# Kernel optimization log

Hardware: AMD Instinct MI355X
Metric: run time of the kernel (lower is better)

The kernel has to match this reference:

```python
import jax, jax.numpy as jnp
import numpy as np

NUM_HEADS = 16
ROPE_BASE = 10000.0


def _rope_cos_sin(seq_len, head_dim, dtype):
    # half-split RoPE tables, shape [1, S, 1, head_dim]
    inv_freq = 1.0 / (ROPE_BASE ** (jnp.arange(0, head_dim, 2, dtype=jnp.float32) / head_dim))
    ang = jnp.arange(seq_len, dtype=jnp.float32)[:, None] * inv_freq[None, :]  # [S, hd/2]
    cos = jnp.concatenate([jnp.cos(ang), jnp.cos(ang)], axis=-1)[None, :, None, :]
    sin = jnp.concatenate([jnp.sin(ang), jnp.sin(ang)], axis=-1)[None, :, None, :]
    return cos.astype(dtype), sin.astype(dtype)


def _rotate_half(t):
    h = t.shape[-1] // 2
    return jnp.concatenate([-t[..., h:], t[..., :h]], axis=-1)


def setup_inputs() -> dict:
    key = jax.random.key(0)
    ks = jax.random.split(key, 5)
    B, S, D = 2, 2048, 1024
    std = 1.0 / np.sqrt(D)
    return {
        "x": jax.random.normal(ks[0], (B, S, D), dtype=jnp.float32),
        "Wqkv": jax.random.normal(ks[1], (D, 3 * D), dtype=jnp.float32) * std,
        "bqkv": jax.random.normal(ks[2], (3 * D,), dtype=jnp.float32) * 0.02,
        "Wproj": jax.random.normal(ks[3], (D, D), dtype=jnp.float32) * std,
        "bproj": jax.random.normal(ks[4], (D,), dtype=jnp.float32) * 0.02,
    }


def reference(x, Wqkv, bqkv, Wproj, bproj):
    B, S, D = x.shape
    H = NUM_HEADS
    hd = D // H
    scale = hd ** (-0.5)

    # fused QKV projection, then split: [B, S, 3, H, hd]
    qkv = (jnp.einsum("bsd,de->bse", x, Wqkv) + bqkv).reshape(B, S, 3, H, hd)
    q, k, v = qkv[:, :, 0], qkv[:, :, 1], qkv[:, :, 2]  # each [B, S, H, hd]

    # rotary embedding on q, k
    cos, sin = _rope_cos_sin(S, hd, x.dtype)
    q = q * cos + _rotate_half(q) * sin
    k = k * cos + _rotate_half(k) * sin

    # scaled dot-product attention (non-causal, matching flash-attn default here)
    scores = jnp.einsum("bqhd,bkhd->bhqk", q, k) * scale  # [B, H, S, S]
    probs = jax.nn.softmax(scores, axis=-1)
    o = jnp.einsum("bhqk,bkhd->bqhd", probs, v).reshape(B, S, D)

    # output projection
    return jnp.einsum("bsd,de->bse", o, Wproj) + bproj
```

## Files before the change

kernel.cpp:

```cpp
#include <hip/hip_runtime.h>

typedef unsigned short u16;
typedef unsigned int   u32;
typedef __bf16 bf16x8 __attribute__((ext_vector_type(8)));
typedef float  f32x4  __attribute__((ext_vector_type(4)));
typedef float  f32x16 __attribute__((ext_vector_type(16)));
typedef u32    u32x4  __attribute__((ext_vector_type(4)));

__device__ __forceinline__ u16 f2bf(float f) {
  u32 u = __builtin_bit_cast(u32, f);
  u += 0x7fffu + ((u >> 16) & 1u);
  return (u16)(u >> 16);
}

#define GLOAD_LDS16(gptr, lptr)                                              \
  __builtin_amdgcn_global_load_lds(                                          \
      (const __attribute__((address_space(1))) void*)(gptr),                 \
      (__attribute__((address_space(3))) void*)(lptr), 16, 0, 0)

#define QK_FOLD 0.18033688011112042f

__global__ __launch_bounds__(256) void prep_kernel(const float* __restrict__ x,
                                                   u16* __restrict__ xb,
                                                   const float* __restrict__ Wq,
                                                   u16* __restrict__ Wqt,
                                                   const float* __restrict__ Wp,
                                                   u16* __restrict__ Wpt,
                                                   float* __restrict__ cost,
                                                   float* __restrict__ sint) {
  __shared__ float tile[32][33];
  const int bid = blockIdx.x;
  if (bid < 4096) {
    const int i = bid * 256 + threadIdx.x;
    const float4 v = ((const float4*)x)[i];
    uint2 o;
    o.x = (u32)f2bf(v.x) | ((u32)f2bf(v.y) << 16);
    o.y = (u32)f2bf(v.z) | ((u32)f2bf(v.w) << 16);
    ((uint2*)xb)[i] = o;
  } else if (bid < 8192) {
    const bool isq = bid < 7168;
    const float* W = isq ? Wq : Wp;
    u16* Wt = isq ? Wqt : Wpt;
    const int t = isq ? (bid - 4096) : (bid - 7168);
    const int ntiles = isq ? 96 : 32;
    const int N = isq ? 3072 : 1024;
    const int k0 = (t / ntiles) * 32, n0 = (t % ntiles) * 32;
    const int tx = threadIdx.x & 31, ty = threadIdx.x >> 5;
#pragma unroll
    for (int i = 0; i < 32; i += 8)
      tile[ty + i][tx] = W[(size_t)(k0 + ty + i) * N + n0 + tx];
    __syncthreads();
#pragma unroll
    for (int i = 0; i < 32; i += 8)
      Wt[(size_t)(n0 + ty + i) * 1024 + k0 + tx] = f2bf(tile[tx][ty + i]);
  } else {
    const int idx = (bid - 8192) * 256 + threadIdx.x;
    const int s = idx >> 5, i = idx & 31;
    float inv = exp2f(-13.287712379549449f * (float)i * (1.0f / 32.0f));
    float sn, cs;
    sincosf((float)s * inv, &sn, &cs);
    cost[idx] = cs;
    sint[idx] = sn;
  }
}

__global__ __launch_bounds__(256) void gemm_qkv_rope_kernel(const u16* __restrict__ A,
                                                            const u16* __restrict__ Bt,
                                                            const float* __restrict__ bias,
                                                            const float* __restrict__ cost,
                                                            const float* __restrict__ sint,
                                                            u16* __restrict__ qb,
                                                            u16* __restrict__ kb,
                                                            u16* __restrict__ vt) {
  __shared__ u16 As[128][64];
  __shared__ u16 Bs[128][64];
  const int bm = blockIdx.y, bn = blockIdx.x;
  const int tid = threadIdx.x;
  const int wave = tid >> 6, lane = tid & 63;
  const int wr = wave >> 1, wc = wave & 1;
  const int l15 = lane & 15, lhi = lane >> 4;
  f32x4 acc[4][4] = {};
  const int K = 1024;

  const size_t arow0 = (size_t)bm * 128, brow0 = (size_t)bn * 128;
  const int srow_in = lane >> 3;
  const int sslot   = (lane & 7) ^ srow_in;

  for (int k0 = 0; k0 < K; k0 += 64) {
#pragma unroll
    for (int i = 0; i < 4; i++) {
      const int r = wave * 32 + i * 8 + srow_in;
      GLOAD_LDS16(A  + (arow0 + r) * K + k0 + sslot * 8, &As[wave * 32 + i * 8][0]);
      GLOAD_LDS16(Bt + (brow0 + r) * K + k0 + sslot * 8, &Bs[wave * 32 + i * 8][0]);
    }
    __syncthreads();

    bf16x8 af[4][2], bfr[4][2];
#pragma unroll
    for (int m = 0; m < 4; m++) {
      const int r = wr * 64 + m * 16 + l15;
#pragma unroll
      for (int kk = 0; kk < 2; kk++)
        af[m][kk] = *(const bf16x8*)(&As[0][0] + r * 64 + (((kk * 4 + lhi) ^ (r & 7)) * 8));
    }
#pragma unroll
    for (int n = 0; n < 4; n++) {
      const int r = wc * 64 + n * 16 + l15;
#pragma unroll
      for (int kk = 0; kk < 2; kk++)
        bfr[n][kk] = *(const bf16x8*)(&Bs[0][0] + r * 64 + (((kk * 4 + lhi) ^ (r & 7)) * 8));
    }
#pragma unroll
    for (int m = 0; m < 4; m++)
#pragma unroll
      for (int n = 0; n < 4; n++) {
        acc[m][n] = __builtin_amdgcn_mfma_f32_16x16x32_bf16(af[m][0], bfr[n][0], acc[m][n], 0, 0, 0);
        acc[m][n] = __builtin_amdgcn_mfma_f32_16x16x32_bf16(af[m][1], bfr[n][1], acc[m][n], 0, 0, 0);
      }
    __syncthreads();
  }

  float bv[4];
#pragma unroll
  for (int n = 0; n < 4; n++) bv[n] = bias[bn * 128 + wc * 64 + n * 16 + l15];

  if (bn < 16) {
    const bool isq = bn < 8;
    u16* dst = isq ? qb : kb;
    const int hcol = bn * 2 + wc - (isq ? 0 : 16);
    const float fold = isq ? QK_FOLD : 1.0f;
#pragma unroll
    for (int m = 0; m < 4; m++)
#pragma unroll
      for (int r = 0; r < 4; r++) {
        const int row = bm * 128 + wr * 64 + m * 16 + lhi * 4 + r;
        const int b = row >> 11, s = row & 2047;
        const float cs0 = cost[s * 32 + l15],      sn0 = sint[s * 32 + l15];
        const float cs1 = cost[s * 32 + 16 + l15], sn1 = sint[s * 32 + 16 + l15];
        const float q0 = acc[m][0][r] + bv[0], q1 = acc[m][2][r] + bv[2];
        const float q2 = acc[m][1][r] + bv[1], q3 = acc[m][3][r] + bv[3];
        u16* orow = dst + ((size_t)(b * 16 + hcol) * 2048 + s) * 64;
        orow[l15]      = f2bf((q0 * cs0 - q1 * sn0) * fold);
        orow[l15 + 32] = f2bf((q1 * cs0 + q0 * sn0) * fold);
        orow[l15 + 16] = f2bf((q2 * cs1 - q3 * sn1) * fold);
        orow[l15 + 48] = f2bf((q3 * cs1 + q2 * sn1) * fold);
      }
  } else {
    const int hcol = bn * 2 + wc - 32;
    const int b = bm >> 4;
#pragma unroll
    for (int n = 0; n < 4; n++) {
      const int d = n * 16 + l15;
      u16* dcol = vt + ((size_t)(b * 16 + hcol) * 64 + d) * 2048;
#pragma unroll
      for (int m = 0; m < 4; m++) {
        const int s = (bm * 128 + wr * 64 + m * 16 + lhi * 4) & 2047;
        uint2 w;
        w.x = (u32)f2bf(acc[m][n][0] + bv[n]) | ((u32)f2bf(acc[m][n][1] + bv[n]) << 16);
        w.y = (u32)f2bf(acc[m][n][2] + bv[n]) | ((u32)f2bf(acc[m][n][3] + bv[n]) << 16);
        *(uint2*)(dcol + s) = w;
      }
    }
  }
}

__global__ __launch_bounds__(256) void gemm_bias_m64_kernel(const u16* __restrict__ A,
                                                            const u16* __restrict__ Bt,
                                                            const float* __restrict__ bias,
                                                            float* __restrict__ C,
                                                            int M, int N, int K) {
  __shared__ u16 As[64][64];
  __shared__ u16 Bs[128][64];
  const int bm = blockIdx.y, bn = blockIdx.x;
  const int tid = threadIdx.x;
  const int wave = tid >> 6, lane = tid & 63;
  const int wr = wave >> 1, wc = wave & 1;
  const int l15 = lane & 15, lhi = lane >> 4;
  f32x4 acc[2][4] = {};

  const size_t arow0 = (size_t)bm * 64, brow0 = (size_t)bn * 128;
  const int srow_in = lane >> 3;
  const int sslot   = (lane & 7) ^ srow_in;

  for (int k0 = 0; k0 < K; k0 += 64) {
#pragma unroll
    for (int i = 0; i < 2; i++) {
      const int r = wave * 16 + i * 8 + srow_in;
      GLOAD_LDS16(A + (arow0 + r) * K + k0 + sslot * 8, &As[wave * 16 + i * 8][0]);
    }
#pragma unroll
    for (int i = 0; i < 4; i++) {
      const int r = wave * 32 + i * 8 + srow_in;
      GLOAD_LDS16(Bt + (brow0 + r) * K + k0 + sslot * 8, &Bs[wave * 32 + i * 8][0]);
    }
    __syncthreads();

    bf16x8 af[2][2], bfr[4][2];
#pragma unroll
    for (int m = 0; m < 2; m++) {
      const int r = wr * 32 + m * 16 + l15;
#pragma unroll
      for (int kk = 0; kk < 2; kk++)
        af[m][kk] = *(const bf16x8*)(&As[0][0] + r * 64 + (((kk * 4 + lhi) ^ (r & 7)) * 8));
    }
#pragma unroll
    for (int n = 0; n < 4; n++) {
      const int r = wc * 64 + n * 16 + l15;
#pragma unroll
      for (int kk = 0; kk < 2; kk++)
        bfr[n][kk] = *(const bf16x8*)(&Bs[0][0] + r * 64 + (((kk * 4 + lhi) ^ (r & 7)) * 8));
    }
#pragma unroll
    for (int m = 0; m < 2; m++)
#pragma unroll
      for (int n = 0; n < 4; n++) {
        acc[m][n] = __builtin_amdgcn_mfma_f32_16x16x32_bf16(af[m][0], bfr[n][0], acc[m][n], 0, 0, 0);
        acc[m][n] = __builtin_amdgcn_mfma_f32_16x16x32_bf16(af[m][1], bfr[n][1], acc[m][n], 0, 0, 0);
      }
    __syncthreads();
  }
#pragma unroll
  for (int n = 0; n < 4; n++) {
    int col = bn * 128 + wc * 64 + n * 16 + l15;
    float bvv = bias[col];
#pragma unroll
    for (int m = 0; m < 2; m++)
#pragma unroll
      for (int r = 0; r < 4; r++) {
        int row = bm * 64 + wr * 32 + m * 16 + lhi * 4 + r;
        C[(size_t)row * N + col] = acc[m][n][r] + bvv;
      }
  }
}

__global__ __launch_bounds__(256) void flash_attn_kernel(const u16* __restrict__ qg,
                                                         const u16* __restrict__ kg,
                                                         const u16* __restrict__ vg,
                                                         u16* __restrict__ og) {
  __shared__ u16 Ks[2][64][64];
  __shared__ u16 Vs[2][64][64];
  const int hw = blockIdx.x;
  const int lb = (hw & 7) * 64 + (hw >> 3);
  const int qt = lb & 15, bh = lb >> 4;
  const int b = bh >> 4, h = bh & 15;
  const int tid = threadIdx.x, wave = tid >> 6, lane = tid & 63;
  const int l5 = lane & 31, hi = lane >> 5;

  const u16* qrow = qg + ((size_t)bh * 2048 + qt * 128 + wave * 32 + l5) * 64 + hi * 8;
  bf16x8 qf[4];
#pragma unroll
  for (int kc = 0; kc < 4; kc++) qf[kc] = *(const bf16x8*)(qrow + kc * 16);

  f32x16 o[2] = {};
  float m_run = -1e30f, l_run = 0.f;

  const u16* gK = kg + (size_t)bh * 2048 * 64;
  const u16* gV = vg + (size_t)bh * 64 * 2048;
  const int srow0 = tid >> 3, sc16 = tid & 7;
  int4 kreg[2], vreg[2];

#pragma unroll
  for (int i = 0; i < 2; i++) {
    int r = srow0 + i * 32;
    kreg[i] = *(const int4*)(gK + (size_t)r * 64 + sc16 * 8);
    vreg[i] = *(const int4*)(gV + (size_t)r * 2048 + sc16 * 8);
  }
#pragma unroll
  for (int i = 0; i < 2; i++) {
    int r = srow0 + i * 32;
    int byo = r * 128 + ((sc16 * 16) ^ ((r & 7) << 4));
    *(int4*)((char*)&Ks[0][0][0] + byo) = kreg[i];
    *(int4*)((char*)&Vs[0][0][0] + byo) = vreg[i];
  }

  for (int kt = 0; kt < 32; kt++) {
    const int cur = kt & 1;
    __syncthreads();
    if (kt < 31) {
#pragma unroll
      for (int i = 0; i < 2; i++) {
        int r = srow0 + i * 32;
        kreg[i] = *(const int4*)(gK + ((size_t)(kt + 1) * 64 + r) * 64 + sc16 * 8);
        vreg[i] = *(const int4*)(gV + (size_t)r * 2048 + (kt + 1) * 64 + sc16 * 8);
      }
    }
    const char* KsB = (const char*)&Ks[cur][0][0];
    const char* VsB = (const char*)&Vs[cur][0][0];

    f32x16 sf[2];
#pragma unroll
    for (int k32 = 0; k32 < 2; k32++) {
      int r = k32 * 32 + l5;
      const char* rowp = KsB + r * 128;
      int sw = (r & 7) << 4;
      f32x16 s = {};
#pragma unroll
      for (int kc = 0; kc < 4; kc++) {
        bf16x8 kf = *(const bf16x8*)(rowp + ((kc * 32 + hi * 16) ^ sw));
        s = __builtin_amdgcn_mfma_f32_32x32x16_bf16(kf, qf[kc], s, 0, 0, 0);
      }
      sf[k32] = s;
    }

    float pmax = sf[0][0];
#pragma unroll
    for (int r = 1; r < 16; r++) pmax = fmaxf(pmax, sf[0][r]);
#pragma unroll
    for (int r = 0; r < 16; r++) pmax = fmaxf(pmax, sf[1][r]);
    pmax = fmaxf(pmax, __shfl_xor(pmax, 32));

    if (!__all(pmax - m_run <= 11.541560327111707f)) {
      float mnew = fmaxf(m_run, pmax);
      float alpha = __builtin_amdgcn_exp2f(m_run - mnew);
      m_run = mnew;
      l_run *= alpha;
#pragma unroll
      for (int dc = 0; dc < 2; dc++)
#pragma unroll
        for (int r = 0; r < 16; r++) o[dc][r] *= alpha;
    }
    float rs = 0.f;
#pragma unroll
    for (int k32 = 0; k32 < 2; k32++)
#pragma unroll
      for (int r = 0; r < 16; r++) {
        float p = __builtin_amdgcn_exp2f(sf[k32][r] - m_run);
        sf[k32][r] = p;
        rs += p;
      }
    rs += __shfl_xor(rs, 32);
    l_run += rs;

    bf16x8 pf[4];
#pragma unroll
    for (int k32 = 0; k32 < 2; k32++) {
      u32 u[8];
#pragma unroll
      for (int m = 0; m < 8; m++) {
        u32 w;
        asm("v_cvt_pk_bf16_f32 %0, %1, %2" : "=v"(w) : "v"(sf[k32][2 * m]), "v"(sf[k32][2 * m + 1]));
        u[m] = w;
      }
      asm("v_permlane32_swap_b32 %0, %1" : "+v"(u[0]), "+v"(u[2]));
      asm("v_permlane32_swap_b32 %0, %1" : "+v"(u[1]), "+v"(u[3]));
      asm("v_permlane32_swap_b32 %0, %1" : "+v"(u[4]), "+v"(u[6]));
      asm("v_permlane32_swap_b32 %0, %1" : "+v"(u[5]), "+v"(u[7]));
      u32x4 w0 = {u[0], u[1], u[2], u[3]};
      u32x4 w1 = {u[4], u[5], u[6], u[7]};
      pf[k32 * 2]     = __builtin_bit_cast(bf16x8, w0);
      pf[k32 * 2 + 1] = __builtin_bit_cast(bf16x8, w1);
    }

#pragma unroll
    for (int dc = 0; dc < 2; dc++) {
      int r = dc * 32 + l5;
      const char* rowp = VsB + r * 128;
      int sw = (r & 7) << 4;
#pragma unroll
      for (int kc = 0; kc < 4; kc++) {
        bf16x8 vf = *(const bf16x8*)(rowp + ((kc * 32 + hi * 16) ^ sw));
        o[dc] = __builtin_amdgcn_mfma_f32_32x32x16_bf16(vf, pf[kc], o[dc], 0, 0, 0);
      }
    }

    if (kt < 31) {
#pragma unroll
      for (int i = 0; i < 2; i++) {
        int r = srow0 + i * 32;
        int byo = r * 128 + ((sc16 * 16) ^ ((r & 7) << 4));
        *(int4*)((char*)&Ks[cur ^ 1][0][0] + byo) = kreg[i];
        *(int4*)((char*)&Vs[cur ^ 1][0][0] + byo) = vreg[i];
      }
    }
  }

  float rinv = 1.0f / l_run;
  int qglob = qt * 128 + wave * 32 + l5;
  u16* orow = og + ((size_t)b * 2048 + qglob) * 1024 + h * 64;
#pragma unroll
  for (int dc = 0; dc < 2; dc++)
#pragma unroll
    for (int m = 0; m < 4; m++) {
      int d0 = dc * 32 + m * 8 + hi * 4;
      float a0 = o[dc][4 * m + 0] * rinv, a1 = o[dc][4 * m + 1] * rinv;
      float a2 = o[dc][4 * m + 2] * rinv, a3 = o[dc][4 * m + 3] * rinv;
      uint2 w;
      w.x = (u32)f2bf(a0) | ((u32)f2bf(a1) << 16);
      w.y = (u32)f2bf(a2) | ((u32)f2bf(a3) << 16);
      *(uint2*)(orow + d0) = w;
    }
}

extern "C" void kernel_launch(void* const* d_in, const int* in_sizes, int n_in,
                              void* d_out, int out_size, void* d_ws, size_t ws_size,
                              hipStream_t stream) {
  const float* x     = (const float*)d_in[0];
  const float* Wqkv  = (const float*)d_in[1];
  const float* bqkv  = (const float*)d_in[2];
  const float* Wproj = (const float*)d_in[3];
  const float* bproj = (const float*)d_in[4];
  float* out = (float*)d_out;

  char* ws = (char*)d_ws;
  u16*   xb    = (u16*)ws;
  u16*   wqkvt = xb + (size_t)4096 * 1024;
  u16*   wprot = wqkvt + (size_t)3072 * 1024;
  float* cost  = (float*)(ws + (size_t)16 * 1024 * 1024);
  float* sint  = cost + 2048 * 32;
  u16*   qb2   = (u16*)(ws + (size_t)64 * 1024 * 1024);
  u16*   kb2   = (u16*)(ws + (size_t)72 * 1024 * 1024);
  u16*   vtw   = (u16*)(ws + (size_t)80 * 1024 * 1024);
  u16*   obw   = (u16*)(ws + (size_t)88 * 1024 * 1024);

  prep_kernel<<<dim3(8448), dim3(256), 0, stream>>>(x, xb, Wqkv, wqkvt, Wproj, wprot, cost, sint);
  gemm_qkv_rope_kernel<<<dim3(24, 32), dim3(256), 0, stream>>>(xb, wqkvt, bqkv, cost, sint,
                                                               qb2, kb2, vtw);
  flash_attn_kernel<<<dim3(512), dim3(256), 0, stream>>>(qb2, kb2, vtw, obw);
  gemm_bias_m64_kernel<<<dim3(8, 64), dim3(256), 0, stream>>>(obw, wprot, bproj, out, 4096, 1024, 1024);
}
```

Measured before the change: 128.1 us.

## Split flash attention keys across two waves with per-wave async LDS staging

The attention kernel now runs 128-thread blocks over 32-query tiles. Each of the two waves handles half of the key sequence in its own LDS slice, and K/V are loaded with global_load_lds in 32-key steps. The waves merge their partial softmax state (m, l, O) through LDS at the end. This removes the per-iteration block barriers and the register round-trip for staging, and it quadruples the grid size for more parallelism. In exchange, each K/V tile is reloaded per 32 queries instead of per 128, which raises L2 traffic, and the waits on global_load_lds are serialized within each wave.

```diff
diff --git a/kernel.cpp b/kernel.cpp
--- a/kernel.cpp
+++ b/kernel.cpp
@@ -233,20 +233,22 @@
   }
 }
 
-__global__ __launch_bounds__(256) void flash_attn_kernel(const u16* __restrict__ qg,
+__global__ __launch_bounds__(128) void flash_attn_kernel(const u16* __restrict__ qg,
                                                          const u16* __restrict__ kg,
                                                          const u16* __restrict__ vg,
                                                          u16* __restrict__ og) {
-  __shared__ u16 Ks[2][64][64];
-  __shared__ u16 Vs[2][64][64];
+  __shared__ __align__(16) char smem[16384];
   const int hw = blockIdx.x;
-  const int lb = (hw & 7) * 64 + (hw >> 3);
-  const int qt = lb & 15, bh = lb >> 4;
+  const int lb = (hw & 7) * 256 + (hw >> 3);
+  const int qt = lb & 63, bh = lb >> 6;
   const int b = bh >> 4, h = bh & 15;
   const int tid = threadIdx.x, wave = tid >> 6, lane = tid & 63;
   const int l5 = lane & 31, hi = lane >> 5;
 
-  const u16* qrow = qg + ((size_t)bh * 2048 + qt * 128 + wave * 32 + l5) * 64 + hi * 8;
+  u16* waveK = (u16*)(smem + wave * 8192);
+  u16* waveV = waveK + 2048;
+
+  const u16* qrow = qg + ((size_t)bh * 2048 + qt * 32 + l5) * 64 + hi * 8;
   bf16x8 qf[4];
 #pragma unroll
   for (int kc = 0; kc < 4; kc++) qf[kc] = *(const bf16x8*)(qrow + kc * 16);
@@ -256,59 +258,55 @@
 
   const u16* gK = kg + (size_t)bh * 2048 * 64;
   const u16* gV = vg + (size_t)bh * 64 * 2048;
-  const int srow0 = tid >> 3, sc16 = tid & 7;
-  int4 kreg[2], vreg[2];
-
-#pragma unroll
-  for (int i = 0; i < 2; i++) {
-    int r = srow0 + i * 32;
-    kreg[i] = *(const int4*)(gK + (size_t)r * 64 + sc16 * 8);
-    vreg[i] = *(const int4*)(gV + (size_t)r * 2048 + sc16 * 8);
-  }
-#pragma unroll
-  for (int i = 0; i < 2; i++) {
-    int r = srow0 + i * 32;
-    int byo = r * 128 + ((sc16 * 16) ^ ((r & 7) << 4));
-    *(int4*)((char*)&Ks[0][0][0] + byo) = kreg[i];
-    *(int4*)((char*)&Vs[0][0][0] + byo) = vreg[i];
-  }
+  const int keybase = wave * 1024;
+  const int srow8 = lane >> 3, kslot = (lane & 7) ^ srow8;
+  const int vrow = lane >> 2, vslot = lane & 3;
+
+#define STAGE_TILE(KT)                                                        \
+  {                                                                           \
+    const int kb_ = keybase + (KT) * 32;                                      \
+    _Pragma("unroll")                                                         \
+    for (int i = 0; i < 4; i++)                                               \
+      GLOAD_LDS16(gK + (size_t)(kb_ + i * 8 + srow8) * 64 + kslot * 8,        \
+                  waveK + i * 512);                                           \
+    _Pragma("unroll")                                                         \
+    for (int i = 0; i < 4; i++)                                               \
+      GLOAD_LDS16(gV + (size_t)(i * 16 + vrow) * 2048 + kb_ + vslot * 8,      \
+                  waveV + i * 512);                                           \
+  }
+
+  STAGE_TILE(0);
 
   for (int kt = 0; kt < 32; kt++) {
-    const int cur = kt & 1;
-    __syncthreads();
-    if (kt < 31) {
-#pragma unroll
-      for (int i = 0; i < 2; i++) {
-        int r = srow0 + i * 32;
-        kreg[i] = *(const int4*)(gK + ((size_t)(kt + 1) * 64 + r) * 64 + sc16 * 8);
-        vreg[i] = *(const int4*)(gV + (size_t)r * 2048 + (kt + 1) * 64 + sc16 * 8);
-      }
-    }
-    const char* KsB = (const char*)&Ks[cur][0][0];
-    const char* VsB = (const char*)&Vs[cur][0][0];
-
-    f32x16 sf[2];
-#pragma unroll
-    for (int k32 = 0; k32 < 2; k32++) {
-      int r = k32 * 32 + l5;
-      const char* rowp = KsB + r * 128;
-      int sw = (r & 7) << 4;
-      f32x16 s = {};
-#pragma unroll
-      for (int kc = 0; kc < 4; kc++) {
-        bf16x8 kf = *(const bf16x8*)(rowp + ((kc * 32 + hi * 16) ^ sw));
-        s = __builtin_amdgcn_mfma_f32_32x32x16_bf16(kf, qf[kc], s, 0, 0, 0);
-      }
-      sf[k32] = s;
-    }
-
-    float pmax = sf[0][0];
-#pragma unroll
-    for (int r = 1; r < 16; r++) pmax = fmaxf(pmax, sf[0][r]);
-#pragma unroll
-    for (int r = 0; r < 16; r++) pmax = fmaxf(pmax, sf[1][r]);
+    asm volatile("s_waitcnt vmcnt(0)" ::: "memory");
+    __builtin_amdgcn_sched_barrier(0);
+
+    bf16x8 kf[4], vf[4];
+#pragma unroll
+    for (int kc = 0; kc < 4; kc++)
+      kf[kc] = *(const bf16x8*)((const char*)waveK + l5 * 128 +
+                                ((kc * 32 + hi * 16) ^ ((l5 & 7) << 4)));
+#pragma unroll
+    for (int dc = 0; dc < 2; dc++)
+#pragma unroll
+      for (int kc = 0; kc < 2; kc++)
+        vf[dc * 2 + kc] = *(const bf16x8*)((const char*)waveV +
+                                           (dc * 32 + l5) * 64 + kc * 32 + hi * 16);
+    asm volatile("s_waitcnt lgkmcnt(0)" ::: "memory");
+    __builtin_amdgcn_sched_barrier(0);
+
+    if (kt < 31) STAGE_TILE(kt + 1);
+    __builtin_amdgcn_sched_barrier(0);
+
+    f32x16 s = {};
+#pragma unroll
+    for (int kc = 0; kc < 4; kc++)
+      s = __builtin_amdgcn_mfma_f32_32x32x16_bf16(kf[kc], qf[kc], s, 0, 0, 0);
+
+    float pmax = s[0];
+#pragma unroll
+    for (int r = 1; r < 16; r++) pmax = fmaxf(pmax, s[r]);
     pmax = fmaxf(pmax, __shfl_xor(pmax, 32));
-
     if (!__all(pmax - m_run <= 11.541560327111707f)) {
       float mnew = fmaxf(m_run, pmax);
       float alpha = __builtin_amdgcn_exp2f(m_run - mnew);
@@ -321,24 +319,21 @@
     }
     float rs = 0.f;
 #pragma unroll
-    for (int k32 = 0; k32 < 2; k32++)
-#pragma unroll
-      for (int r = 0; r < 16; r++) {
-        float p = __builtin_amdgcn_exp2f(sf[k32][r] - m_run);
-        sf[k32][r] = p;
-        rs += p;
-      }
+    for (int r = 0; r < 16; r++) {
+      float p = __builtin_amdgcn_exp2f(s[r] - m_run);
+      s[r] = p;
+      rs += p;
+    }
     rs += __shfl_xor(rs, 32);
     l_run += rs;
 
-    bf16x8 pf[4];
-#pragma unroll
-    for (int k32 = 0; k32 < 2; k32++) {
+    bf16x8 pf[2];
+    {
       u32 u[8];
 #pragma unroll
       for (int m = 0; m < 8; m++) {
         u32 w;
-        asm("v_cvt_pk_bf16_f32 %0, %1, %2" : "=v"(w) : "v"(sf[k32][2 * m]), "v"(sf[k32][2 * m + 1]));
+        asm("v_cvt_pk_bf16_f32 %0, %1, %2" : "=v"(w) : "v"(s[2 * m]), "v"(s[2 * m + 1]));
         u[m] = w;
       }
       asm("v_permlane32_swap_b32 %0, %1" : "+v"(u[0]), "+v"(u[2]));
@@ -347,48 +342,61 @@
       asm("v_permlane32_swap_b32 %0, %1" : "+v"(u[5]), "+v"(u[7]));
       u32x4 w0 = {u[0], u[1], u[2], u[3]};
       u32x4 w1 = {u[4], u[5], u[6], u[7]};
-      pf[k32 * 2]     = __builtin_bit_cast(bf16x8, w0);
-      pf[k32 * 2 + 1] = __builtin_bit_cast(bf16x8, w1);
-    }
-
-#pragma unroll
-    for (int dc = 0; dc < 2; dc++) {
-      int r = dc * 32 + l5;
-      const char* rowp = VsB + r * 128;
-      int sw = (r & 7) << 4;
-#pragma unroll
-      for (int kc = 0; kc < 4; kc++) {
-        bf16x8 vf = *(const bf16x8*)(rowp + ((kc * 32 + hi * 16) ^ sw));
-        o[dc] = __builtin_amdgcn_mfma_f32_32x32x16_bf16(vf, pf[kc], o[dc], 0, 0, 0);
-      }
-    }
-
-    if (kt < 31) {
-#pragma unroll
-      for (int i = 0; i < 2; i++) {
-        int r = srow0 + i * 32;
-        int byo = r * 128 + ((sc16 * 16) ^ ((r & 7) << 4));
-        *(int4*)((char*)&Ks[cur ^ 1][0][0] + byo) = kreg[i];
-        *(int4*)((char*)&Vs[cur ^ 1][0][0] + byo) = vreg[i];
-      }
-    }
-  }
-
-  float rinv = 1.0f / l_run;
-  int qglob = qt * 128 + wave * 32 + l5;
-  u16* orow = og + ((size_t)b * 2048 + qglob) * 1024 + h * 64;
-#pragma unroll
-  for (int dc = 0; dc < 2; dc++)
-#pragma unroll
-    for (int m = 0; m < 4; m++) {
-      int d0 = dc * 32 + m * 8 + hi * 4;
-      float a0 = o[dc][4 * m + 0] * rinv, a1 = o[dc][4 * m + 1] * rinv;
-      float a2 = o[dc][4 * m + 2] * rinv, a3 = o[dc][4 * m + 3] * rinv;
-      uint2 w;
-      w.x = (u32)f2bf(a0) | ((u32)f2bf(a1) << 16);
-      w.y = (u32)f2bf(a2) | ((u32)f2bf(a3) << 16);
-      *(uint2*)(orow + d0) = w;
-    }
+      pf[0] = __builtin_bit_cast(bf16x8, w0);
+      pf[1] = __builtin_bit_cast(bf16x8, w1);
+    }
+
+#pragma unroll
+    for (int dc = 0; dc < 2; dc++)
+#pragma unroll
+      for (int kc = 0; kc < 2; kc++)
+        o[dc] = __builtin_amdgcn_mfma_f32_32x32x16_bf16(vf[dc * 2 + kc], pf[kc], o[dc], 0, 0, 0);
+  }
+#undef STAGE_TILE
+
+  float* Ob = (float*)smem;
+  float* Mv = (float*)(smem + 8192);
+  float* Lv = Mv + 32;
+
+  __syncthreads();
+  if (wave == 1) {
+    if (hi == 0) { Mv[l5] = m_run; Lv[l5] = l_run; }
+#pragma unroll
+    for (int dc = 0; dc < 2; dc++)
+#pragma unroll
+      for (int m = 0; m < 4; m++) {
+        const int c = dc * 8 + m * 2 + hi;
+        float4 w = {o[dc][4 * m + 0], o[dc][4 * m + 1],
+                    o[dc][4 * m + 2], o[dc][4 * m + 3]};
+        *(float4*)(Ob + l5 * 64 + (c ^ (l5 & 15)) * 4) = w;
+      }
+  }
+  __syncthreads();
+  if (wave == 0) {
+    const float m1 = Mv[l5], l1 = Lv[l5];
+    const float M = fmaxf(m_run, m1);
+    const float a0 = __builtin_amdgcn_exp2f(m_run - M);
+    const float a1 = __builtin_amdgcn_exp2f(m1 - M);
+    const float rinv = 1.0f / (l_run * a0 + l1 * a1);
+    const int qglob = qt * 32 + l5;
+    u16* orow = og + ((size_t)b * 2048 + qglob) * 1024 + h * 64;
+#pragma unroll
+    for (int dc = 0; dc < 2; dc++)
+#pragma unroll
+      for (int m = 0; m < 4; m++) {
+        const int c = dc * 8 + m * 2 + hi;
+        const float4 o1 = *(const float4*)(Ob + l5 * 64 + (c ^ (l5 & 15)) * 4);
+        const int d0 = dc * 32 + m * 8 + hi * 4;
+        float a = (o[dc][4 * m + 0] * a0 + o1.x * a1) * rinv;
+        float bvv = (o[dc][4 * m + 1] * a0 + o1.y * a1) * rinv;
+        float cvv = (o[dc][4 * m + 2] * a0 + o1.z * a1) * rinv;
+        float dvv = (o[dc][4 * m + 3] * a0 + o1.w * a1) * rinv;
+        uint2 w;
+        w.x = (u32)f2bf(a) | ((u32)f2bf(bvv) << 16);
+        w.y = (u32)f2bf(cvv) | ((u32)f2bf(dvv) << 16);
+        *(uint2*)(orow + d0) = w;
+      }
+  }
 }
 
 extern "C" void kernel_launch(void* const* d_in, const int* in_sizes, int n_in,
@@ -415,6 +423,6 @@
   prep_kernel<<<dim3(8448), dim3(256), 0, stream>>>(x, xb, Wqkv, wqkvt, Wproj, wprot, cost, sint);
   gemm_qkv_rope_kernel<<<dim3(24, 32), dim3(256), 0, stream>>>(xb, wqkvt, bqkv, cost, sint,
                                                                qb2, kb2, vtw);
-  flash_attn_kernel<<<dim3(512), dim3(256), 0, stream>>>(qb2, kb2, vtw, obw);
+  flash_attn_kernel<<<dim3(2048), dim3(128), 0, stream>>>(qb2, kb2, vtw, obw);
   gemm_bias_m64_kernel<<<dim3(8, 64), dim3(256), 0, stream>>>(obw, wprot, bproj, out, 4096, 1024, 1024);
 }
```

Result: slower. 154.1 us (+20.3%).

## Split flash attention over KV halves and merge partials in new kernel

Applied to the files above, without the earlier changes.

Splits each attention block's key/value range into two halves, doubling the grid from 512 to 1024 blocks. Each half writes unnormalized fp32 partial outputs plus its running max and sum, and a new merge kernel combines them with a log-sum-exp rescale and writes bf16. The aim is better occupancy across the MI355X's CUs, since 512 blocks underfill 256 CUs. The cost is an extra launch and roughly 32MB of fp32 partial writes and reads.

```diff
diff --git a/kernel.cpp b/kernel.cpp
--- a/kernel.cpp
+++ b/kernel.cpp
@@ -236,13 +236,13 @@
 __global__ __launch_bounds__(256) void flash_attn_kernel(const u16* __restrict__ qg,
                                                          const u16* __restrict__ kg,
                                                          const u16* __restrict__ vg,
-                                                         u16* __restrict__ og) {
+                                                         float* __restrict__ opart,
+                                                         float* __restrict__ ml) {
   __shared__ u16 Ks[2][64][64];
   __shared__ u16 Vs[2][64][64];
   const int hw = blockIdx.x;
-  const int lb = (hw & 7) * 64 + (hw >> 3);
-  const int qt = lb & 15, bh = lb >> 4;
-  const int b = bh >> 4, h = bh & 15;
+  const int lb = (hw & 7) * 128 + (hw >> 3);
+  const int part = lb & 1, qt = (lb >> 1) & 15, bh = lb >> 5;
   const int tid = threadIdx.x, wave = tid >> 6, lane = tid & 63;
   const int l5 = lane & 31, hi = lane >> 5;
 
@@ -257,13 +257,14 @@
   const u16* gK = kg + (size_t)bh * 2048 * 64;
   const u16* gV = vg + (size_t)bh * 64 * 2048;
   const int srow0 = tid >> 3, sc16 = tid & 7;
+  const int kt0 = part * 16, kt1 = kt0 + 16;
   int4 kreg[2], vreg[2];
 
 #pragma unroll
   for (int i = 0; i < 2; i++) {
     int r = srow0 + i * 32;
-    kreg[i] = *(const int4*)(gK + (size_t)r * 64 + sc16 * 8);
-    vreg[i] = *(const int4*)(gV + (size_t)r * 2048 + sc16 * 8);
+    kreg[i] = *(const int4*)(gK + ((size_t)kt0 * 64 + r) * 64 + sc16 * 8);
+    vreg[i] = *(const int4*)(gV + (size_t)r * 2048 + kt0 * 64 + sc16 * 8);
   }
 #pragma unroll
   for (int i = 0; i < 2; i++) {
@@ -273,10 +274,10 @@
     *(int4*)((char*)&Vs[0][0][0] + byo) = vreg[i];
   }
 
-  for (int kt = 0; kt < 32; kt++) {
+  for (int kt = kt0; kt < kt1; kt++) {
     const int cur = kt & 1;
     __syncthreads();
-    if (kt < 31) {
+    if (kt < kt1 - 1) {
 #pragma unroll
       for (int i = 0; i < 2; i++) {
         int r = srow0 + i * 32;
@@ -363,7 +364,7 @@
       }
     }
 
-    if (kt < 31) {
+    if (kt < kt1 - 1) {
 #pragma unroll
       for (int i = 0; i < 2; i++) {
         int r = srow0 + i * 32;
@@ -374,21 +375,61 @@
     }
   }
 
-  float rinv = 1.0f / l_run;
-  int qglob = qt * 128 + wave * 32 + l5;
-  u16* orow = og + ((size_t)b * 2048 + qglob) * 1024 + h * 64;
+  const int qglob = qt * 128 + wave * 32 + l5;
+  const size_t idx = ((size_t)part * 32 + bh) * 2048 + qglob;
+  float* orow = opart + idx * 64;
 #pragma unroll
   for (int dc = 0; dc < 2; dc++)
 #pragma unroll
     for (int m = 0; m < 4; m++) {
-      int d0 = dc * 32 + m * 8 + hi * 4;
-      float a0 = o[dc][4 * m + 0] * rinv, a1 = o[dc][4 * m + 1] * rinv;
-      float a2 = o[dc][4 * m + 2] * rinv, a3 = o[dc][4 * m + 3] * rinv;
-      uint2 w;
-      w.x = (u32)f2bf(a0) | ((u32)f2bf(a1) << 16);
-      w.y = (u32)f2bf(a2) | ((u32)f2bf(a3) << 16);
-      *(uint2*)(orow + d0) = w;
-    }
+      const int d0 = dc * 32 + m * 8 + hi * 4;
+      float4 w = {o[dc][4 * m + 0], o[dc][4 * m + 1],
+                  o[dc][4 * m + 2], o[dc][4 * m + 3]};
+      *(float4*)(orow + d0) = w;
+    }
+  if (hi == 0) {
+    float2 p = {m_run, l_run};
+    ((float2*)ml)[idx] = p;
+  }
+}
+
+__global__ __launch_bounds__(256) void flash_merge_kernel(const float* __restrict__ opart,
+                                                          const float* __restrict__ ml,
+                                                          u16* __restrict__ og) {
+  const int t = blockIdx.x * 256 + threadIdx.x;
+  const int d0 = (t & 3) * 16;
+  const int q  = (t >> 2) & 2047;
+  const int bh = t >> 13;
+  const int b = bh >> 4, h = bh & 15;
+  const size_t idx = (size_t)bh * 2048 + q;
+  const size_t pstride = (size_t)32 * 2048;
+
+  const float2 p0 = ((const float2*)ml)[idx];
+  const float2 p1 = ((const float2*)ml)[pstride + idx];
+  const float M = fmaxf(p0.x, p1.x);
+  const float a0 = __builtin_amdgcn_exp2f(p0.x - M);
+  const float a1 = __builtin_amdgcn_exp2f(p1.x - M);
+  const float rinv = 1.0f / (p0.y * a0 + p1.y * a1);
+
+  const float* o0 = opart + idx * 64 + d0;
+  const float* o1 = opart + (pstride + idx) * 64 + d0;
+  u32 w[8];
+#pragma unroll
+  for (int j = 0; j < 4; j++) {
+    const float4 x0 = *(const float4*)(o0 + j * 4);
+    const float4 x1 = *(const float4*)(o1 + j * 4);
+    const float v0 = (x0.x * a0 + x1.x * a1) * rinv;
+    const float v1 = (x0.y * a0 + x1.y * a1) * rinv;
+    const float v2 = (x0.z * a0 + x1.z * a1) * rinv;
+    const float v3 = (x0.w * a0 + x1.w * a1) * rinv;
+    w[j * 2]     = (u32)f2bf(v0) | ((u32)f2bf(v1) << 16);
+    w[j * 2 + 1] = (u32)f2bf(v2) | ((u32)f2bf(v3) << 16);
+  }
+  u16* orow = og + ((size_t)b * 2048 + q) * 1024 + h * 64 + d0;
+  u32x4 wa = {w[0], w[1], w[2], w[3]};
+  u32x4 wb = {w[4], w[5], w[6], w[7]};
+  *(u32x4*)(orow) = wa;
+  *(u32x4*)(orow + 8) = wb;
 }
 
 extern "C" void kernel_launch(void* const* d_in, const int* in_sizes, int n_in,
@@ -407,6 +448,8 @@
   u16*   wprot = wqkvt + (size_t)3072 * 1024;
   float* cost  = (float*)(ws + (size_t)16 * 1024 * 1024);
   float* sint  = cost + 2048 * 32;
+  float* opart = (float*)(ws + (size_t)24 * 1024 * 1024);
+  float* mlbuf = (float*)(ws + (size_t)56 * 1024 * 1024);
   u16*   qb2   = (u16*)(ws + (size_t)64 * 1024 * 1024);
   u16*   kb2   = (u16*)(ws + (size_t)72 * 1024 * 1024);
   u16*   vtw   = (u16*)(ws + (size_t)80 * 1024 * 1024);
@@ -415,6 +458,7 @@
   prep_kernel<<<dim3(8448), dim3(256), 0, stream>>>(x, xb, Wqkv, wqkvt, Wproj, wprot, cost, sint);
   gemm_qkv_rope_kernel<<<dim3(24, 32), dim3(256), 0, stream>>>(xb, wqkvt, bqkv, cost, sint,
                                                                qb2, kb2, vtw);
-  flash_attn_kernel<<<dim3(512), dim3(256), 0, stream>>>(qb2, kb2, vtw, obw);
+  flash_attn_kernel<<<dim3(1024), dim3(256), 0, stream>>>(qb2, kb2, vtw, opart, mlbuf);
+  flash_merge_kernel<<<dim3(1024), dim3(256), 0, stream>>>(opart, mlbuf, obw);
   gemm_bias_m64_kernel<<<dim3(8, 64), dim3(256), 0, stream>>>(obw, wprot, bproj, out, 4096, 1024, 1024);
 }
```

After: 165.5 us. 1.29x slower.
